# Kernel tuning notes

Hardware: AMD Instinct MI355X
Metric: run time of the kernel (lower is better)

The kernel has to match this reference:

```python
import jax, jax.numpy as jnp
import numpy as np

N_USERS = 100_000
N_ITEMS = 150_000
N_REL = 16
N_FACT = 4
D = 64
N_EDGES = 2_000_000
NNZ = 2_000_000
N_LAYERS = 2


def setup_inputs() -> dict:
    key = jax.random.key(0)
    ks = jax.random.split(key, 10)
    return {
        "user_emb": jax.random.normal(ks[0], (N_USERS, D), jnp.float32) * 0.1,
        "entity_emb": jax.random.normal(ks[1], (N_ITEMS, D), jnp.float32) * 0.1,
        "latent_emb": jax.random.normal(ks[2], (N_FACT, D), jnp.float32) * 0.1,
        "weight": jax.random.normal(ks[3], (N_REL, D), jnp.float32) * 0.1,
        "disen_weight_att": jax.random.normal(ks[4], (N_FACT, N_REL), jnp.float32) * 0.1,
        "interact_val": jax.random.uniform(ks[5], (NNZ,), jnp.float32),
        "edge_index": jax.random.randint(ks[6], (2, N_EDGES), 0, N_ITEMS),
        "edge_type": jax.random.randint(ks[7], (N_EDGES,), 1, N_REL + 1),
        "interact_row": jax.random.randint(ks[8], (NNZ,), 0, N_USERS),
        "interact_col": jax.random.randint(ks[9], (NNZ,), 0, N_ITEMS),
    }


def _dist_corr(t1, t2):
    # torch _distance_correlation on 1-D vectors of length n
    n = t1.shape[0]
    t1 = t1[:, None]
    t2 = t2[:, None]
    dx = jnp.sqrt(jnp.maximum(t1 ** 2 - 2.0 * (t1 @ t1.T) + (t1 ** 2).T, 0.0) + 1e-8)
    dy = jnp.sqrt(jnp.maximum(t2 ** 2 - 2.0 * (t2 @ t2.T) + (t2 ** 2).T, 0.0) + 1e-8)
    A = dx - dx.mean(0, keepdims=True) - dx.mean(1, keepdims=True) + dx.mean()
    B = dy - dy.mean(0, keepdims=True) - dy.mean(1, keepdims=True) + dy.mean()
    dcov = lambda P, Q: jnp.sqrt(jnp.maximum((P * Q).sum() / (n * n), 0.0) + 1e-8)
    return dcov(A, B) / jnp.sqrt(dcov(A, A) * dcov(B, B) + 1e-8)


def _l2_normalize(x):
    # F.normalize(x) default: dim=1, eps=1e-12
    nrm = jnp.sqrt(jnp.sum(x * x, axis=1, keepdims=True))
    return x / jnp.maximum(nrm, 1e-12)


def _forward(user_emb, entity_emb, latent_emb, weight, disen_weight_att,
             interact_val, edge_index, edge_type, interact_row, interact_col):
    head, tail = edge_index[0], edge_index[1]
    entity_res, user_res = entity_emb, user_emb

    # correlation score over disentangled factor pairs (n_factors small, fixed loop)
    cor = jnp.asarray(0.0, jnp.float32)
    for i in range(N_FACT):
        for j in range(i + 1, N_FACT):
            cor = cor + _dist_corr(disen_weight_att[i], disen_weight_att[j])

    ones_e = jnp.ones((N_EDGES,), entity_emb.dtype)
    cnt = jax.ops.segment_sum(ones_e, head, num_segments=N_ITEMS)  # [n_items]
    denom = jnp.maximum(cnt, 1.0)[:, None]

    for _ in range(N_LAYERS):
        # KG aggregate: gather + elementwise mul + scatter_mean
        msg = entity_emb[tail] * weight[edge_type - 1]            # [E, D]
        entity_agg = jax.ops.segment_sum(msg, head, num_segments=N_ITEMS) / denom

        # user->factor attention
        score = jax.nn.softmax(user_emb @ latent_emb.T, axis=1)[..., None]  # [U, F, 1]

        # sparse mm: user_agg = interact_mat @ entity_emb
        user_agg = jax.ops.segment_sum(interact_val[:, None] * entity_emb[interact_col],
                                       interact_row, num_segments=N_USERS)  # [U, D]

        dis = jax.nn.softmax(disen_weight_att, axis=-1) @ weight  # [F, D]
        mix = (dis[None, :, :] * score).sum(axis=1)               # [U, D]
        user_agg = user_agg * mix + user_agg

        entity_emb = _l2_normalize(entity_agg)
        user_emb = _l2_normalize(user_agg)
        entity_res = entity_res + entity_emb
        user_res = user_res + user_emb

    return entity_res, user_res, cor


def reference(user_emb, entity_emb, latent_emb, weight, disen_weight_att,
              interact_val, edge_index, edge_type, interact_row, interact_col):
    return _forward(user_emb, entity_emb, latent_emb, weight, disen_weight_att,
                    interact_val, edge_index, edge_type, interact_row, interact_col)
```

## Files before the change

kernel.cpp:

```cpp
#include <hip/hip_runtime.h>

#define N_USERS 100000
#define N_ITEMS 150000
#define N_REL 16
#define N_FACT 4
#define DD 64
#define N_EDGES 2000000
#define NNZ 2000000

#define KE 293
#define KU 196
#define TBE 4096
#define TBU 2048
#define GEB ((N_EDGES + TBE - 1) / TBE)
#define GUB ((NNZ + TBU - 1) / TBU)
#define EBLK2 ((N_ITEMS + 31) / 32)
#define UBLK2 (N_USERS / 32)
#define LGRID 2048
#define IBLK ((N_ITEMS * 16 + 255) / 256)
#define CAPE 8192
#define CAPU 12288

typedef float          __attribute__((ext_vector_type(4))) f32x4;
typedef unsigned short __attribute__((ext_vector_type(8))) u16x8;

__device__ __forceinline__ unsigned short f2b(float f) {
    unsigned u = __float_as_uint(f);
    return (unsigned short)((u + 0x7FFFu + ((u >> 16) & 1u)) >> 16);
}
__device__ __forceinline__ float b2f(unsigned short h) {
    return __uint_as_float((unsigned)h << 16);
}


struct BinSME {
    unsigned int stage[TBE];
    unsigned short sbkt[TBE];
    int hist[KE];
    int lofs[KE + 1];
    int gbase[KE];
};
struct BinSMU {
    unsigned long long stage[TBU];
    unsigned short sbkt[TBU];
    int hist[KU];
    int lofs[KU + 1];
    int gbase[KU];
};

__global__ __launch_bounds__(256) void prologue_kernel(const float4* __restrict__ uemb,
                                                       const float4* __restrict__ eemb,
                                                       ushort4* __restrict__ entB0_u4,
                                                       float4* __restrict__ cur_usr,
                                                       float4* __restrict__ eres,
                                                       float4* __restrict__ ures,
                                                       const float* __restrict__ att,
                                                       const float* __restrict__ weight,
                                                       float* __restrict__ cor_out,
                                                       float* __restrict__ dis,
                                                       const int* __restrict__ eidx,
                                                       const int* __restrict__ etype,
                                                       const int* __restrict__ irow,
                                                       const int* __restrict__ icol,
                                                       const float* __restrict__ ival,
                                                       int* __restrict__ bktcntE,
                                                       int* __restrict__ bktcntU,
                                                       unsigned int* __restrict__ binE,
                                                       unsigned long long* __restrict__ binU) {
    __shared__ union { BinSME e; BinSMU u; } sm;
    __shared__ float sA[256], sB[256];
    __shared__ float srx[16], scx[16], sry[16], scy[16];
    __shared__ float stotx, stoty;
    int tid = threadIdx.x;
    int bid = blockIdx.x;
    if (bid < GEB) {
        int e0 = bid * TBE;
        int nloc = min(TBE, N_EDGES - e0);
        for (int b = tid; b < KE; b += 256) sm.e.hist[b] = 0;
        __syncthreads();
        for (int i = tid; i < nloc; i += 256)
            atomicAdd(&sm.e.hist[__builtin_nontemporal_load(&eidx[e0 + i]) >> 9], 1);
        __syncthreads();
        if (tid < 64) {
            const int chunk = (KE + 63) >> 6;
            int base = tid * chunk;
            int s = 0;
            for (int c = 0; c < chunk; ++c) { int ix = base + c; if (ix < KE) s += sm.e.hist[ix]; }
            int inc = s;
            for (int d = 1; d < 64; d <<= 1) { int tv = __shfl_up(inc, d, 64); if (tid >= d) inc += tv; }
            int run = inc - s;
            for (int c = 0; c < chunk; ++c) { int ix = base + c; if (ix < KE) { sm.e.lofs[ix] = run; run += sm.e.hist[ix]; } }
            if (tid == 63) sm.e.lofs[KE] = run;
        }
        __syncthreads();
        for (int b = tid; b < KE; b += 256) {
            int cnt = sm.e.lofs[b + 1] - sm.e.lofs[b];
            if (cnt > 0) sm.e.gbase[b] = atomicAdd(&bktcntE[b], cnt);
            sm.e.hist[b] = sm.e.lofs[b];
        }
        __syncthreads();
        for (int i = tid; i < nloc; i += 256) {
            int h = __builtin_nontemporal_load(&eidx[e0 + i]);
            int tt = __builtin_nontemporal_load(&eidx[N_EDGES + e0 + i]);
            int r  = __builtin_nontemporal_load(&etype[e0 + i]) - 1;
            int b = h >> 9;
            int slot = atomicAdd(&sm.e.hist[b], 1);
            sm.e.stage[slot] = (unsigned int)tt | ((unsigned int)r << 18) | ((unsigned int)(h & 511) << 22);
            sm.e.sbkt[slot] = (unsigned short)b;
        }
        __syncthreads();
        int total = sm.e.lofs[KE];
        for (int i = tid; i < total; i += 256) {
            int b = sm.e.sbkt[i];
            int slot = sm.e.gbase[b] + (i - sm.e.lofs[b]);
            if (slot < CAPE) binE[(size_t)b * CAPE + slot] = sm.e.stage[i];
        }
    } else if (bid < GEB + GUB) {
        int e0 = (bid - GEB) * TBU;
        int nloc = min(TBU, NNZ - e0);
        for (int b = tid; b < KU; b += 256) sm.u.hist[b] = 0;
        __syncthreads();
        for (int i = tid; i < nloc; i += 256)
            atomicAdd(&sm.u.hist[__builtin_nontemporal_load(&irow[e0 + i]) >> 9], 1);
        __syncthreads();
        if (tid < 64) {
            const int chunk = (KU + 63) >> 6;
            int base = tid * chunk;
            int s = 0;
            for (int c = 0; c < chunk; ++c) { int ix = base + c; if (ix < KU) s += sm.u.hist[ix]; }
            int inc = s;
            for (int d = 1; d < 64; d <<= 1) { int tv = __shfl_up(inc, d, 64); if (tid >= d) inc += tv; }
            int run = inc - s;
            for (int c = 0; c < chunk; ++c) { int ix = base + c; if (ix < KU) { sm.u.lofs[ix] = run; run += sm.u.hist[ix]; } }
            if (tid == 63) sm.u.lofs[KU] = run;
        }
        __syncthreads();
        for (int b = tid; b < KU; b += 256) {
            int cnt = sm.u.lofs[b + 1] - sm.u.lofs[b];
            if (cnt > 0) sm.u.gbase[b] = atomicAdd(&bktcntU[b], cnt);
            sm.u.hist[b] = sm.u.lofs[b];
        }
        __syncthreads();
        for (int i = tid; i < nloc; i += 256) {
            int row = __builtin_nontemporal_load(&irow[e0 + i]);
            int col = __builtin_nontemporal_load(&icol[e0 + i]);
            float v  = __builtin_nontemporal_load(&ival[e0 + i]);
            int b = row >> 9;
            int slot = atomicAdd(&sm.u.hist[b], 1);
            sm.u.stage[slot] = ((unsigned long long)__float_as_uint(v) << 32)
                             | ((unsigned long long)(row & 511) << 18)
                             | (unsigned int)col;
            sm.u.sbkt[slot] = (unsigned short)b;
        }
        __syncthreads();
        int total = sm.u.lofs[KU];
        for (int i = tid; i < total; i += 256) {
            int b = sm.u.sbkt[i];
            int slot = sm.u.gbase[b] + (i - sm.u.lofs[b]);
            if (slot < CAPU) binU[(size_t)b * CAPU + slot] = sm.u.stage[i];
        }
    } else if (bid < GEB + GUB + 2) {
        int sb = bid - (GEB + GUB);
        int t = tid;
        if (sb == 1) {
            int f = t >> 6, d = t & 63;
            float m = -1e30f;
            for (int r = 0; r < N_REL; ++r) m = fmaxf(m, att[f * N_REL + r]);
            float w[N_REL]; float s = 0.f;
            for (int r = 0; r < N_REL; ++r) { w[r] = expf(att[f * N_REL + r] - m); s += w[r]; }
            float acc = 0.f;
            for (int r = 0; r < N_REL; ++r) acc += (w[r] / s) * weight[r * DD + d];
            dis[f * DD + d] = acc;
            return;
        }
        int a = t >> 4, b = t & 15;
        float cor_acc = 0.f;
        for (int i = 0; i < N_FACT; ++i) {
            for (int j = i + 1; j < N_FACT; ++j) {
                const float* t1 = att + i * N_REL;
                const float* t2 = att + j * N_REL;
                float d1 = t1[a] - t1[b];
                float d2 = t2[a] - t2[b];
                float dx = sqrtf(d1 * d1 + 1e-8f);
                float dy = sqrtf(d2 * d2 + 1e-8f);
                sA[t] = dx; sB[t] = dy;
                __syncthreads();
                if (t < 16)      { float s = 0; for (int k = 0; k < 16; ++k) s += sA[t * 16 + k]; srx[t] = s; }
                else if (t < 32) { int c = t & 15; float s = 0; for (int k = 0; k < 16; ++k) s += sA[k * 16 + c]; scx[c] = s; }
                else if (t < 48) { int r = t & 15; float s = 0; for (int k = 0; k < 16; ++k) s += sB[r * 16 + k]; sry[r] = s; }
                else if (t < 64) { int c = t & 15; float s = 0; for (int k = 0; k < 16; ++k) s += sB[k * 16 + c]; scy[c] = s; }
                __syncthreads();
                if (t == 0)  { float s = 0; for (int k = 0; k < 16; ++k) s += srx[k]; stotx = s; }
                if (t == 64) { float s = 0; for (int k = 0; k < 16; ++k) s += sry[k]; stoty = s; }
                __syncthreads();
                float A = dx - scx[b] * 0.0625f - srx[a] * 0.0625f + stotx * (1.f / 256.f);
                float B = dy - scy[b] * 0.0625f - sry[a] * 0.0625f + stoty * (1.f / 256.f);
                float vab = A * B, vaa = A * A, vbb = B * B;
                for (int off = 32; off; off >>= 1) {
                    vab += __shfl_xor(vab, off, 64);
                    vaa += __shfl_xor(vaa, off, 64);
                    vbb += __shfl_xor(vbb, off, 64);
                }
                __syncthreads();
                if ((t & 63) == 0) {
                    int w = t >> 6;
                    sA[w] = vab; sA[4 + w] = vaa; sA[8 + w] = vbb;
                }
                __syncthreads();
                if (t == 0) {
                    float sAB = sA[0] + sA[1] + sA[2] + sA[3];
                    float sAA = sA[4] + sA[5] + sA[6] + sA[7];
                    float sBB = sA[8] + sA[9] + sA[10] + sA[11];
                    float dab = sqrtf(fmaxf(sAB * (1.f / 256.f), 0.f) + 1e-8f);
                    float daa = sqrtf(fmaxf(sAA * (1.f / 256.f), 0.f) + 1e-8f);
                    float dbb = sqrtf(fmaxf(sBB * (1.f / 256.f), 0.f) + 1e-8f);
                    cor_acc += dab / sqrtf(daa * dbb + 1e-8f);
                }
                __syncthreads();
            }
        }
        if (t == 0) *cor_out = cor_acc;
    } else {
        int i = (bid - (GEB + GUB + 2)) * 256 + tid;
        const int NE4 = N_ITEMS * 16;
        const int NU4 = N_USERS * 16;
        if (i < NE4) {
            float4 v = eemb[i];
            eres[i] = v;
            int rr = i >> 4, f = i & 15;
            entB0_u4[(size_t)rr * 16 + ((f & 7) << 1) + (f >> 3)] =
                make_ushort4(f2b(v.x), f2b(v.y), f2b(v.z), f2b(v.w));
        }
        if (i < NU4) { float4 v = uemb[i]; cur_usr[i] = v; ures[i] = v; }
    }
}

__global__ __launch_bounds__(512) void bucket_scan_kernel(const int* __restrict__ bktcntE,
                                                          const int* __restrict__ bktcntU,
                                                          int* __restrict__ bbaseE,
                                                          int* __restrict__ bbaseU,
                                                          int* __restrict__ eoff,
                                                          int* __restrict__ uoff) {
    __shared__ int lds[512];
    int t = threadIdx.x;
    const int* cnt; int* bbase; int K; int* off; int n; int cap;
    if (blockIdx.x == 0) { cnt = bktcntE; bbase = bbaseE; K = KE; off = eoff; n = N_ITEMS; cap = CAPE; }
    else                 { cnt = bktcntU; bbase = bbaseU; K = KU; off = uoff; n = N_USERS; cap = CAPU; }
    int v = (t < K) ? min(cnt[t], cap) : 0;
    lds[t] = v; __syncthreads();
    for (int o = 1; o < 512; o <<= 1) {
        int add = (t >= o) ? lds[t - o] : 0;
        __syncthreads();
        lds[t] += add;
        __syncthreads();
    }
    if (t < K) bbase[t] = lds[t] - v;
    if (t == K - 1) off[n] = lds[t];
}

__global__ __launch_bounds__(256) void fine_both_kernel(const int* __restrict__ bktcntE,
                                                        const int* __restrict__ bktcntU,
                                                        const int* __restrict__ bbaseE,
                                                        const int* __restrict__ bbaseU,
                                                        const unsigned int* __restrict__ binE,
                                                        const unsigned long long* __restrict__ binU,
                                                        int* __restrict__ eoff,
                                                        int* __restrict__ uoff,
                                                        int* __restrict__ pack,
                                                        unsigned long long* __restrict__ upair) {
    __shared__ int hist[512];
    __shared__ int scanb[256];
    __shared__ int curs[512];
    int tid = threadIdx.x;
    if (blockIdx.x < KE) {
        int b = blockIdx.x;
        int row0 = b << 9;
        int cnt = min(bktcntE[b], CAPE);
        int base = bbaseE[b];
        for (int r = tid; r < 512; r += 256) hist[r] = 0;
        __syncthreads();
        for (int i = tid; i < cnt; i += 256)
            atomicAdd(&hist[binE[(size_t)b * CAPE + i] >> 22], 1);
        __syncthreads();
        int a0 = hist[2 * tid], a1 = hist[2 * tid + 1];
        int s = a0 + a1;
        scanb[tid] = s; __syncthreads();
        for (int o = 1; o < 256; o <<= 1) {
            int add = (tid >= o) ? scanb[tid - o] : 0;
            __syncthreads();
            scanb[tid] += add;
            __syncthreads();
        }
        int excl = scanb[tid] - s;
        curs[2 * tid]     = base + excl;
        curs[2 * tid + 1] = base + excl + a0;
        int row = row0 + 2 * tid;
        if (row < N_ITEMS)     eoff[row]     = base + excl;
        if (row + 1 < N_ITEMS) eoff[row + 1] = base + excl + a0;
        __syncthreads();
        for (int i = tid; i < cnt; i += 256) {
            unsigned int p = binE[(size_t)b * CAPE + i];
            int pos = atomicAdd(&curs[p >> 22], 1);
            pack[pos] = (int)(p & 0x3FFFFF);
        }
    } else {
        int b = blockIdx.x - KE;
        int row0 = b << 9;
        int cnt = min(bktcntU[b], CAPU);
        int base = bbaseU[b];
        for (int r = tid; r < 512; r += 256) hist[r] = 0;
        __syncthreads();
        for (int i = tid; i < cnt; i += 256)
            atomicAdd(&hist[(int)(binU[(size_t)b * CAPU + i] >> 18) & 511], 1);
        __syncthreads();
        int a0 = hist[2 * tid], a1 = hist[2 * tid + 1];
        int s = a0 + a1;
        scanb[tid] = s; __syncthreads();
        for (int o = 1; o < 256; o <<= 1) {
            int add = (tid >= o) ? scanb[tid - o] : 0;
            __syncthreads();
            scanb[tid] += add;
            __syncthreads();
        }
        int excl = scanb[tid] - s;
        curs[2 * tid]     = base + excl;
        curs[2 * tid + 1] = base + excl + a0;
        int row = row0 + 2 * tid;
        if (row < N_USERS)     uoff[row]     = base + excl;
        if (row + 1 < N_USERS) uoff[row + 1] = base + excl + a0;
        __syncthreads();
        for (int i = tid; i < cnt; i += 256) {
            unsigned long long p = binU[(size_t)b * CAPU + i];
            int pos = atomicAdd(&curs[(int)(p >> 18) & 511], 1);
            upair[pos] = p & 0xFFFFFFFF0003FFFFull;
        }
    }
}

__global__ __launch_bounds__(256) void layer_kernel(const int* __restrict__ eoff,
                                                    const int* __restrict__ pack,
                                                    const int* __restrict__ uoff,
                                                    const unsigned long long* __restrict__ upair,
                                                    const u16x8* __restrict__ entBIn,
                                                    const float4* __restrict__ w4,
                                                    const float4* __restrict__ lat4,
                                                    const float4* __restrict__ dis4,
                                                    u16x8* __restrict__ entBOut,
                                                    float4* __restrict__ eres4,
                                                    float4* __restrict__ usr4,
                                                    float4* __restrict__ ures4) {
    int w = threadIdx.x >> 6;
    int lane = threadIdx.x & 63;
    int g = lane >> 3, li = lane & 7;
    for (int tile = blockIdx.x; tile < EBLK2 + UBLK2; tile += LGRID) {
    if (tile < EBLK2) {
        int row = tile * 32 + w * 8 + g;
        bool valid = row < N_ITEMS;
        int beg = 0, deg = 0;
        if (valid) { beg = eoff[row]; deg = eoff[row + 1] - beg; }
        int mdeg = deg;
        for (int o = 8; o < 64; o <<= 1) mdeg = max(mdeg, __shfl_xor(mdeg, o, 64));
        float4 a0 = make_float4(0.f, 0.f, 0.f, 0.f);
        float4 a1 = make_float4(0.f, 0.f, 0.f, 0.f);
        for (int cb = 0; cb < mdeg; cb += 8) {
            int pk = 0;
            if (cb + li < deg) pk = __builtin_nontemporal_load(&pack[beg + cb + li]);
            int pv[8];
            #pragma unroll
            for (int k = 0; k < 8; ++k) pv[k] = __shfl(pk, k, 8);
            u16x8 rows[8];
            #pragma unroll
            for (int k = 0; k < 8; ++k)
                rows[k] = entBIn[(size_t)(pv[k] & 0x3FFFF) * 8 + li];
            #pragma unroll
            for (int k = 0; k < 8; ++k) {
                if (cb + k < deg) {
                    int r = pv[k] >> 18;
                    float4 wa = w4[r * 16 + li];
                    float4 wb = w4[r * 16 + 8 + li];
                    a0.x += b2f(rows[k][0]) * wa.x; a0.y += b2f(rows[k][1]) * wa.y;
                    a0.z += b2f(rows[k][2]) * wa.z; a0.w += b2f(rows[k][3]) * wa.w;
                    a1.x += b2f(rows[k][4]) * wb.x; a1.y += b2f(rows[k][5]) * wb.y;
                    a1.z += b2f(rows[k][6]) * wb.z; a1.w += b2f(rows[k][7]) * wb.w;
                }
            }
        }
        if (valid) {
            float inv = 1.f / fmaxf((float)deg, 1.f);
            a0.x *= inv; a0.y *= inv; a0.z *= inv; a0.w *= inv;
            a1.x *= inv; a1.y *= inv; a1.z *= inv; a1.w *= inv;
            float ss = a0.x * a0.x + a0.y * a0.y + a0.z * a0.z + a0.w * a0.w
                     + a1.x * a1.x + a1.y * a1.y + a1.z * a1.z + a1.w * a1.w;
            for (int o = 4; o; o >>= 1) ss += __shfl_xor(ss, o, 8);
            float rn = 1.f / fmaxf(sqrtf(ss), 1e-12f);
            a0.x *= rn; a0.y *= rn; a0.z *= rn; a0.w *= rn;
            a1.x *= rn; a1.y *= rn; a1.z *= rn; a1.w *= rn;
            u16x8 ob;
            ob[0] = f2b(a0.x); ob[1] = f2b(a0.y); ob[2] = f2b(a0.z); ob[3] = f2b(a0.w);
            ob[4] = f2b(a1.x); ob[5] = f2b(a1.y); ob[6] = f2b(a1.z); ob[7] = f2b(a1.w);
            entBOut[(size_t)row * 8 + li] = ob;
            float4 r0 = eres4[(size_t)row * 16 + li];
            float4 r1 = eres4[(size_t)row * 16 + 8 + li];
            r0.x += a0.x; r0.y += a0.y; r0.z += a0.z; r0.w += a0.w;
            r1.x += a1.x; r1.y += a1.y; r1.z += a1.z; r1.w += a1.w;
            eres4[(size_t)row * 16 + li]     = r0;
            eres4[(size_t)row * 16 + 8 + li] = r1;
        }
    } else {
        int u = (tile - EBLK2) * 32 + w * 8 + g;
        float4 uv0 = usr4[(size_t)u * 16 + li];
        float4 uv1 = usr4[(size_t)u * 16 + 8 + li];
        float p0, p1, p2, p3;
        {
            float4 la = lat4[0 * 16 + li], lb = lat4[0 * 16 + 8 + li];
            p0 = uv0.x * la.x + uv0.y * la.y + uv0.z * la.z + uv0.w * la.w
               + uv1.x * lb.x + uv1.y * lb.y + uv1.z * lb.z + uv1.w * lb.w;
        }
        {
            float4 la = lat4[1 * 16 + li], lb = lat4[1 * 16 + 8 + li];
            p1 = uv0.x * la.x + uv0.y * la.y + uv0.z * la.z + uv0.w * la.w
               + uv1.x * lb.x + uv1.y * lb.y + uv1.z * lb.z + uv1.w * lb.w;
        }
        {
            float4 la = lat4[2 * 16 + li], lb = lat4[2 * 16 + 8 + li];
            p2 = uv0.x * la.x + uv0.y * la.y + uv0.z * la.z + uv0.w * la.w
               + uv1.x * lb.x + uv1.y * lb.y + uv1.z * lb.z + uv1.w * lb.w;
        }
        {
            float4 la = lat4[3 * 16 + li], lb = lat4[3 * 16 + 8 + li];
            p3 = uv0.x * la.x + uv0.y * la.y + uv0.z * la.z + uv0.w * la.w
               + uv1.x * lb.x + uv1.y * lb.y + uv1.z * lb.z + uv1.w * lb.w;
        }
        for (int o = 4; o; o >>= 1) {
            p0 += __shfl_xor(p0, o, 8);
            p1 += __shfl_xor(p1, o, 8);
            p2 += __shfl_xor(p2, o, 8);
            p3 += __shfl_xor(p3, o, 8);
        }
        float m = fmaxf(fmaxf(p0, p1), fmaxf(p2, p3));
        float e0 = expf(p0 - m), e1 = expf(p1 - m), e2 = expf(p2 - m), e3 = expf(p3 - m);
        float sinv = 1.f / (e0 + e1 + e2 + e3);
        float s0 = e0 * sinv, s1 = e1 * sinv, s2 = e2 * sinv, s3 = e3 * sinv;
        float4 mix0, mix1;
        {
            float4 d0a = dis4[0 * 16 + li], d1a = dis4[1 * 16 + li];
            float4 d2a = dis4[2 * 16 + li], d3a = dis4[3 * 16 + li];
            mix0 = make_float4(d0a.x * s0 + d1a.x * s1 + d2a.x * s2 + d3a.x * s3,
                               d0a.y * s0 + d1a.y * s1 + d2a.y * s2 + d3a.y * s3,
                               d0a.z * s0 + d1a.z * s1 + d2a.z * s2 + d3a.z * s3,
                               d0a.w * s0 + d1a.w * s1 + d2a.w * s2 + d3a.w * s3);
            float4 d0b = dis4[0 * 16 + 8 + li], d1b = dis4[1 * 16 + 8 + li];
            float4 d2b = dis4[2 * 16 + 8 + li], d3b = dis4[3 * 16 + 8 + li];
            mix1 = make_float4(d0b.x * s0 + d1b.x * s1 + d2b.x * s2 + d3b.x * s3,
                               d0b.y * s0 + d1b.y * s1 + d2b.y * s2 + d3b.y * s3,
                               d0b.z * s0 + d1b.z * s1 + d2b.z * s2 + d3b.z * s3,
                               d0b.w * s0 + d1b.w * s1 + d2b.w * s2 + d3b.w * s3);
        }
        int beg = uoff[u];
        int deg = uoff[u + 1] - beg;
        int mdeg = deg;
        for (int o = 8; o < 64; o <<= 1) mdeg = max(mdeg, __shfl_xor(mdeg, o, 64));
        float4 a0 = make_float4(0.f, 0.f, 0.f, 0.f);
        float4 a1 = make_float4(0.f, 0.f, 0.f, 0.f);
        for (int cb = 0; cb < mdeg; cb += 8) {
            unsigned long long pr = 0;
            if (cb + li < deg) pr = __builtin_nontemporal_load(&upair[beg + cb + li]);
            int clo[8]; float cval[8];
            #pragma unroll
            for (int k = 0; k < 8; ++k) {
                clo[k]  = __shfl((int)(pr & 0xFFFFFFFFu), k, 8);
                cval[k] = __uint_as_float((unsigned)__shfl((int)(pr >> 32), k, 8));
            }
            u16x8 rows[8];
            #pragma unroll
            for (int k = 0; k < 8; ++k)
                rows[k] = entBIn[(size_t)clo[k] * 8 + li];
            #pragma unroll
            for (int k = 0; k < 8; ++k) {
                float cv = cval[k];
                a0.x += cv * b2f(rows[k][0]); a0.y += cv * b2f(rows[k][1]);
                a0.z += cv * b2f(rows[k][2]); a0.w += cv * b2f(rows[k][3]);
                a1.x += cv * b2f(rows[k][4]); a1.y += cv * b2f(rows[k][5]);
                a1.z += cv * b2f(rows[k][6]); a1.w += cv * b2f(rows[k][7]);
            }
        }
        float4 v0 = make_float4(a0.x * mix0.x + a0.x, a0.y * mix0.y + a0.y,
                                a0.z * mix0.z + a0.z, a0.w * mix0.w + a0.w);
        float4 v1 = make_float4(a1.x * mix1.x + a1.x, a1.y * mix1.y + a1.y,
                                a1.z * mix1.z + a1.z, a1.w * mix1.w + a1.w);
        float ss = v0.x * v0.x + v0.y * v0.y + v0.z * v0.z + v0.w * v0.w
                 + v1.x * v1.x + v1.y * v1.y + v1.z * v1.z + v1.w * v1.w;
        for (int o = 4; o; o >>= 1) ss += __shfl_xor(ss, o, 8);
        float rn = 1.f / fmaxf(sqrtf(ss), 1e-12f);
        v0.x *= rn; v0.y *= rn; v0.z *= rn; v0.w *= rn;
        v1.x *= rn; v1.y *= rn; v1.z *= rn; v1.w *= rn;
        usr4[(size_t)u * 16 + li]     = v0;
        usr4[(size_t)u * 16 + 8 + li] = v1;
        float4 r0 = ures4[(size_t)u * 16 + li];
        float4 r1 = ures4[(size_t)u * 16 + 8 + li];
        r0.x += v0.x; r0.y += v0.y; r0.z += v0.z; r0.w += v0.w;
        r1.x += v1.x; r1.y += v1.y; r1.z += v1.z; r1.w += v1.w;
        ures4[(size_t)u * 16 + li]     = r0;
        ures4[(size_t)u * 16 + 8 + li] = r1;
    }
    }
}

extern "C" void kernel_launch(void* const* d_in, const int* in_sizes, int n_in,
                              void* d_out, int out_size, void* d_ws, size_t ws_size,
                              hipStream_t stream) {
    const float* user_emb   = (const float*)d_in[0];
    const float* entity_emb = (const float*)d_in[1];
    const float* latent     = (const float*)d_in[2];
    const float* weight     = (const float*)d_in[3];
    const float* att        = (const float*)d_in[4];
    const float* ival       = (const float*)d_in[5];
    const int*   eidx       = (const int*)d_in[6];
    const int*   etype      = (const int*)d_in[7];
    const int*   irow       = (const int*)d_in[8];
    const int*   icol       = (const int*)d_in[9];

    float* out        = (float*)d_out;
    float* entity_res = out;
    float* user_res   = out + (size_t)N_ITEMS * DD;
    float* cor_out    = out + (size_t)N_ITEMS * DD + (size_t)N_USERS * DD;

    char* ws = (char*)d_ws;
    char* entB0 = ws;               ws += (size_t)N_ITEMS * DD * 2;
    char* entB1 = ws;               ws += (size_t)N_ITEMS * DD * 2;
    float* cur_usr = (float*)ws;    ws += (size_t)N_USERS * DD * 4;
    int*   eoff    = (int*)ws;      ws += (size_t)(N_ITEMS + 1) * 4;
    int*   epack   = (int*)ws;      ws += (size_t)N_EDGES * 4;
    int*   uoff    = (int*)ws;      ws += (size_t)(N_USERS + 1) * 4;
    unsigned long long* upair = (unsigned long long*)ws; ws += (size_t)NNZ * 8;
    unsigned long long* binU  = (unsigned long long*)ws; ws += (size_t)KU * CAPU * 8;
    int*   bktcntE = (int*)ws;      ws += 512 * 4;
    int*   bktcntU = (int*)ws;      ws += 512 * 4;
    int*   bbaseE  = (int*)ws;      ws += 512 * 4;
    int*   bbaseU  = (int*)ws;      ws += 512 * 4;
    float* dis     = (float*)ws;    ws += 256 * 4;
    unsigned int* binE = (unsigned int*)entB1;

    hipMemsetAsync(bktcntE, 0, 512 * 4, stream);
    hipMemsetAsync(bktcntU, 0, 512 * 4, stream);

    prologue_kernel<<<GEB + GUB + 2 + IBLK, 256, 0, stream>>>(
        (const float4*)user_emb, (const float4*)entity_emb,
        (ushort4*)entB0, (float4*)cur_usr, (float4*)entity_res, (float4*)user_res,
        att, weight, cor_out, dis,
        eidx, etype, irow, icol, ival,
        bktcntE, bktcntU, binE, binU);

    bucket_scan_kernel<<<2, 512, 0, stream>>>(bktcntE, bktcntU, bbaseE, bbaseU, eoff, uoff);
    fine_both_kernel<<<KE + KU, 256, 0, stream>>>(bktcntE, bktcntU, bbaseE, bbaseU,
                                                  binE, binU, eoff, uoff, epack, upair);

    char* entbuf[2] = { entB0, entB1 };
    for (int layer = 0; layer < 2; ++layer) {
        char* eIn  = entbuf[layer & 1];
        char* eOut = entbuf[(layer & 1) ^ 1];
        layer_kernel<<<LGRID, 256, 0, stream>>>(eoff, epack, uoff, upair,
                                                (const u16x8*)eIn,
                                                (const float4*)weight,
                                                (const float4*)latent,
                                                (const float4*)dis,
                                                (u16x8*)eOut,
                                                (float4*)entity_res,
                                                (float4*)cur_usr,
                                                (float4*)user_res);
    }
}
```

Measured before the change: 387.9 us.

## Defer residual sums to an epilogue using saved bf16 layer outputs

```diff
diff --git a/kernel.cpp b/kernel.cpp
--- a/kernel.cpp
+++ b/kernel.cpp
@@ -16,7 +16,6 @@
 #define GUB ((NNZ + TBU - 1) / TBU)
 #define EBLK2 ((N_ITEMS + 31) / 32)
 #define UBLK2 (N_USERS / 32)
-#define LGRID 2048
 #define IBLK ((N_ITEMS * 16 + 255) / 256)
 #define CAPE 8192
 #define CAPU 12288
@@ -30,6 +29,9 @@
 }
 __device__ __forceinline__ float b2f(unsigned short h) {
     return __uint_as_float((unsigned)h << 16);
+}
+__device__ __forceinline__ float4 b4fu(ushort4 r) {
+    return make_float4(b2f(r.x), b2f(r.y), b2f(r.z), b2f(r.w));
 }
 
 
@@ -52,8 +54,6 @@
                                                        const float4* __restrict__ eemb,
                                                        ushort4* __restrict__ entB0_u4,
                                                        float4* __restrict__ cur_usr,
-                                                       float4* __restrict__ eres,
-                                                       float4* __restrict__ ures,
                                                        const float* __restrict__ att,
                                                        const float* __restrict__ weight,
                                                        float* __restrict__ cor_out,
@@ -226,12 +226,11 @@
         const int NU4 = N_USERS * 16;
         if (i < NE4) {
             float4 v = eemb[i];
-            eres[i] = v;
             int rr = i >> 4, f = i & 15;
             entB0_u4[(size_t)rr * 16 + ((f & 7) << 1) + (f >> 3)] =
                 make_ushort4(f2b(v.x), f2b(v.y), f2b(v.z), f2b(v.w));
         }
-        if (i < NU4) { float4 v = uemb[i]; cur_usr[i] = v; ures[i] = v; }
+        if (i < NU4) cur_usr[i] = uemb[i];
     }
 }
 
@@ -346,15 +345,14 @@
                                                     const float4* __restrict__ lat4,
                                                     const float4* __restrict__ dis4,
                                                     u16x8* __restrict__ entBOut,
-                                                    float4* __restrict__ eres4,
                                                     float4* __restrict__ usr4,
-                                                    float4* __restrict__ ures4) {
+                                                    u16x8* __restrict__ u1out,
+                                                    int save_u1) {
     int w = threadIdx.x >> 6;
     int lane = threadIdx.x & 63;
     int g = lane >> 3, li = lane & 7;
-    for (int tile = blockIdx.x; tile < EBLK2 + UBLK2; tile += LGRID) {
-    if (tile < EBLK2) {
-        int row = tile * 32 + w * 8 + g;
+    if (blockIdx.x < EBLK2) {
+        int row = blockIdx.x * 32 + w * 8 + g;
         bool valid = row < N_ITEMS;
         int beg = 0, deg = 0;
         if (valid) { beg = eoff[row]; deg = eoff[row + 1] - beg; }
@@ -399,15 +397,9 @@
             ob[0] = f2b(a0.x); ob[1] = f2b(a0.y); ob[2] = f2b(a0.z); ob[3] = f2b(a0.w);
             ob[4] = f2b(a1.x); ob[5] = f2b(a1.y); ob[6] = f2b(a1.z); ob[7] = f2b(a1.w);
             entBOut[(size_t)row * 8 + li] = ob;
-            float4 r0 = eres4[(size_t)row * 16 + li];
-            float4 r1 = eres4[(size_t)row * 16 + 8 + li];
-            r0.x += a0.x; r0.y += a0.y; r0.z += a0.z; r0.w += a0.w;
-            r1.x += a1.x; r1.y += a1.y; r1.z += a1.z; r1.w += a1.w;
-            eres4[(size_t)row * 16 + li]     = r0;
-            eres4[(size_t)row * 16 + 8 + li] = r1;
         }
     } else {
-        int u = (tile - EBLK2) * 32 + w * 8 + g;
+        int u = (blockIdx.x - EBLK2) * 32 + w * 8 + g;
         float4 uv0 = usr4[(size_t)u * 16 + li];
         float4 uv1 = usr4[(size_t)u * 16 + 8 + li];
         float p0, p1, p2, p3;
@@ -496,13 +488,43 @@
         v1.x *= rn; v1.y *= rn; v1.z *= rn; v1.w *= rn;
         usr4[(size_t)u * 16 + li]     = v0;
         usr4[(size_t)u * 16 + 8 + li] = v1;
-        float4 r0 = ures4[(size_t)u * 16 + li];
-        float4 r1 = ures4[(size_t)u * 16 + 8 + li];
-        r0.x += v0.x; r0.y += v0.y; r0.z += v0.z; r0.w += v0.w;
-        r1.x += v1.x; r1.y += v1.y; r1.z += v1.z; r1.w += v1.w;
-        ures4[(size_t)u * 16 + li]     = r0;
-        ures4[(size_t)u * 16 + 8 + li] = r1;
+        if (save_u1) {
+            u16x8 ob;
+            ob[0] = f2b(v0.x); ob[1] = f2b(v0.y); ob[2] = f2b(v0.z); ob[3] = f2b(v0.w);
+            ob[4] = f2b(v1.x); ob[5] = f2b(v1.y); ob[6] = f2b(v1.z); ob[7] = f2b(v1.w);
+            u1out[(size_t)u * 8 + li] = ob;
+        }
     }
+}
+
+__global__ __launch_bounds__(256) void epilogue_kernel(const float4* __restrict__ eemb,
+                                                       const float4* __restrict__ uemb,
+                                                       const ushort4* __restrict__ e1u4,
+                                                       const ushort4* __restrict__ e2u4,
+                                                       const ushort4* __restrict__ u1u4,
+                                                       const float4* __restrict__ cur_usr,
+                                                       float4* __restrict__ eres,
+                                                       float4* __restrict__ ures) {
+    int i = blockIdx.x * 256 + threadIdx.x;
+    const int NE4 = N_ITEMS * 16;
+    const int NU4 = N_USERS * 16;
+    if (i < NE4) {
+        int rr = i >> 4, f = i & 15;
+        size_t pidx = (size_t)rr * 16 + ((f & 7) << 1) + (f >> 3);
+        float4 base = eemb[i];
+        float4 x1 = b4fu(e1u4[pidx]);
+        float4 x2 = b4fu(e2u4[pidx]);
+        eres[i] = make_float4(base.x + x1.x + x2.x, base.y + x1.y + x2.y,
+                              base.z + x1.z + x2.z, base.w + x1.w + x2.w);
+    }
+    if (i < NU4) {
+        int rr = i >> 4, f = i & 15;
+        size_t pidx = (size_t)rr * 16 + ((f & 7) << 1) + (f >> 3);
+        float4 base = uemb[i];
+        float4 x1 = b4fu(u1u4[pidx]);
+        float4 x2 = cur_usr[i];
+        ures[i] = make_float4(base.x + x1.x + x2.x, base.y + x1.y + x2.y,
+                              base.z + x1.z + x2.z, base.w + x1.w + x2.w);
     }
 }
 
@@ -528,6 +550,7 @@
     char* ws = (char*)d_ws;
     char* entB0 = ws;               ws += (size_t)N_ITEMS * DD * 2;
     char* entB1 = ws;               ws += (size_t)N_ITEMS * DD * 2;
+    char* u1b   = ws;               ws += (size_t)N_USERS * DD * 2;
     float* cur_usr = (float*)ws;    ws += (size_t)N_USERS * DD * 4;
     int*   eoff    = (int*)ws;      ws += (size_t)(N_ITEMS + 1) * 4;
     int*   epack   = (int*)ws;      ws += (size_t)N_EDGES * 4;
@@ -546,7 +569,7 @@
 
     prologue_kernel<<<GEB + GUB + 2 + IBLK, 256, 0, stream>>>(
         (const float4*)user_emb, (const float4*)entity_emb,
-        (ushort4*)entB0, (float4*)cur_usr, (float4*)entity_res, (float4*)user_res,
+        (ushort4*)entB0, (float4*)cur_usr,
         att, weight, cor_out, dis,
         eidx, etype, irow, icol, ival,
         bktcntE, bktcntU, binE, binU);
@@ -555,18 +578,29 @@
     fine_both_kernel<<<KE + KU, 256, 0, stream>>>(bktcntE, bktcntU, bbaseE, bbaseU,
                                                   binE, binU, eoff, uoff, epack, upair);
 
-    char* entbuf[2] = { entB0, entB1 };
-    for (int layer = 0; layer < 2; ++layer) {
-        char* eIn  = entbuf[layer & 1];
-        char* eOut = entbuf[(layer & 1) ^ 1];
-        layer_kernel<<<LGRID, 256, 0, stream>>>(eoff, epack, uoff, upair,
-                                                (const u16x8*)eIn,
-                                                (const float4*)weight,
-                                                (const float4*)latent,
-                                                (const float4*)dis,
-                                                (u16x8*)eOut,
-                                                (float4*)entity_res,
-                                                (float4*)cur_usr,
-                                                (float4*)user_res);
-    }
-}
+    layer_kernel<<<EBLK2 + UBLK2, 256, 0, stream>>>(eoff, epack, uoff, upair,
+                                                    (const u16x8*)entB0,
+                                                    (const float4*)weight,
+                                                    (const float4*)latent,
+                                                    (const float4*)dis,
+                                                    (u16x8*)entB1,
+                                                    (float4*)cur_usr,
+                                                    (u16x8*)u1b, 1);
+    layer_kernel<<<EBLK2 + UBLK2, 256, 0, stream>>>(eoff, epack, uoff, upair,
+                                                    (const u16x8*)entB1,
+                                                    (const float4*)weight,
+                                                    (const float4*)latent,
+                                                    (const float4*)dis,
+                                                    (u16x8*)entB0,
+                                                    (float4*)cur_usr,
+                                                    (u16x8*)u1b, 0);
+
+    epilogue_kernel<<<IBLK, 256, 0, stream>>>((const float4*)entity_emb,
+                                              (const float4*)user_emb,
+                                              (const ushort4*)entB1,
+                                              (const ushort4*)entB0,
+                                              (const ushort4*)u1b,
+                                              (const float4*)cur_usr,
+                                              (float4*)entity_res,
+                                              (float4*)user_res);
+}
```

Result: faster. 371.7 us (-4.2%).
